# Optimization experiments

Hardware: AMD Instinct MI355X
Metric: run time of the kernel (lower is better)

## Reference

```python
import jax, jax.numpy as jnp
import numpy as np

B, T, D = 16, 512, 256
HS, D_A, R = 512, 64, 8


def setup_inputs() -> dict:
    key = jax.random.key(0)
    ks = jax.random.split(key, 8)
    s = lambda *sh: 1.0 / np.sqrt(sh[0])
    x = jax.random.normal(ks[0], (B, T, D), dtype=jnp.float32)
    w_first = jax.random.normal(ks[1], (D, D_A), dtype=jnp.float32) * s(D)
    b_first = jnp.zeros((D_A,), dtype=jnp.float32)
    w_second = jax.random.normal(ks[2], (D_A, R), dtype=jnp.float32) * s(D_A)
    b_second = jnp.zeros((R,), dtype=jnp.float32)
    weight_iBarh = jax.random.normal(ks[3], (D, 4 * HS), dtype=jnp.float32) * s(D)
    weight_hh = jax.random.normal(ks[4], (HS, 4 * HS), dtype=jnp.float32) * s(HS)
    bias = jnp.zeros((4 * HS,), dtype=jnp.float32)
    return {"x": x, "w_first": w_first, "b_first": b_first,
            "w_second": w_second, "b_second": b_second,
            "weight_iBarh": weight_iBarh, "weight_hh": weight_hh, "bias": bias}


def _forward(x, w_first, b_first, w_second, b_second, weight_iBarh, weight_hh, bias):
    b, t, d = x.shape
    hs = weight_hh.shape[0]
    r = w_second.shape[1]
    # attention logits for every timestep: (B, T, r)
    s = jnp.tanh(x @ w_first + b_first) @ w_second + b_second
    # causal mask: query t attends to keys j <= t
    mask = jnp.tril(jnp.ones((t, t), dtype=bool))  # (t_query, j_key)
    # logits: (B, Tq, Tk, r); softmax over key axis per (t, r), masked to prefix
    logits = jnp.where(mask[None, :, :, None], s[:, None, :, :], -jnp.inf)
    attn = jax.nn.softmax(logits, axis=2).mean(axis=-1)  # (B, Tq, Tk) == mean over r
    # M_t = attention-weighted average of prefix inputs: (B, T, D)
    M = jnp.einsum('btj,bjd->btd', attn, x)
    gates_x = jnp.einsum('btd,dg->btg', M, weight_iBarh) + bias  # (B, T, 4H)

    def step(carry, gx):
        h, c = carry
        g = gx + h @ weight_hh  # (B, 4H)
        i = jax.nn.sigmoid(g[:, :hs])
        f = jax.nn.sigmoid(g[:, hs:2 * hs])
        gg = jnp.tanh(g[:, 2 * hs:3 * hs])
        o = jax.nn.sigmoid(g[:, 3 * hs:])
        c = f * c + i * gg
        h = o * jnp.tanh(c)
        return (h, c), h

    h0 = jnp.zeros((b, hs), dtype=x.dtype)
    c0 = jnp.zeros((b, hs), dtype=x.dtype)
    (h_t, c_t), hseq = jax.lax.scan(step, (h0, c0), jnp.swapaxes(gates_x, 0, 1))
    hidden_seq = jnp.swapaxes(hseq, 0, 1)  # (B, T, H)
    return hidden_seq, h_t, c_t


def reference(x, w_first, b_first, w_second, b_second, weight_iBarh, weight_hh, bias):
    return _forward(x, w_first, b_first, w_second, b_second, weight_iBarh, weight_hh, bias)
```

## Files before the change

kernel.cpp:

```cpp
#include <hip/hip_runtime.h>
#include <math.h>

#define BB 16
#define TT 512
#define DD 256
#define HS 512
#define DA 64
#define RR 8
#define G4H 2048

typedef __attribute__((ext_vector_type(2))) float f2;
typedef __attribute__((ext_vector_type(8))) short bf16x8;
typedef __attribute__((ext_vector_type(4))) float f32x4;
typedef unsigned short ushort_t;


__device__ __forceinline__ ushort_t f2bf(float f) {
  const unsigned u = __float_as_uint(f);
  return (ushort_t)((u + 0x7FFFu + ((u >> 16) & 1u)) >> 16);
}

__global__ __launch_bounds__(256) void k0w_transpose(
    const float* __restrict__ W, ushort_t* __restrict__ Wt) {
  __shared__ float tl[64][65];
  const int kb = (blockIdx.x & 3) * 64;
  const int nb = (blockIdx.x >> 2) * 64;
  const int tid = threadIdx.x;
  for (int i = tid; i < 4096; i += 256)
    tl[i >> 6][i & 63] = W[(kb + (i >> 6)) * 2048 + nb + (i & 63)];
  __syncthreads();
  for (int i = tid; i < 4096; i += 256) {
    const int n = i >> 6, k = i & 63;
    Wt[(nb + n) * 256 + kb + k] = f2bf(tl[k][n]);
  }
}

__global__ __launch_bounds__(256) void k1_score(
    const float* __restrict__ x, const float* __restrict__ w1,
    const float* __restrict__ b1, const float* __restrict__ w2,
    const float* __restrict__ b2, float* __restrict__ s_out) {
  const int wave = threadIdx.x >> 6;
  const int lane = threadIdx.x & 63;
  for (int i = 0; i < 4; ++i) {
    const int bt = blockIdx.x * 16 + wave * 4 + i;
    const float* xr = x + bt * DD;
    float acc = b1[lane];
    #pragma unroll 4
    for (int d = 0; d < DD; ++d)
      acc = fmaf(xr[d], w1[d * DA + lane], acc);
    const float a = tanhf(acc);
    #pragma unroll
    for (int r = 0; r < RR; ++r) {
      float v = a * w2[lane * RR + r];
      for (int off = 32; off > 0; off >>= 1) v += __shfl_xor(v, off);
      if (lane == 0) s_out[bt * RR + r] = v + b2[r];
    }
  }
}

__global__ __launch_bounds__(512) void k2_prefix(
    const float* __restrict__ s_in, float* __restrict__ e_out,
    float* __restrict__ inv_out) {
  const int b = blockIdx.x >> 3, r = blockIdx.x & 7;
  const int t = threadIdx.x;
  __shared__ float red[TT];
  __shared__ float buf[2][TT];
  const float v = s_in[(b * TT + t) * RR + r];
  red[t] = v;
  __syncthreads();
  for (int off = 256; off >= 1; off >>= 1) {
    if (t < off) red[t] = fmaxf(red[t], red[t + off]);
    __syncthreads();
  }
  const float m = red[0];
  const float e = expf(v - m);
  int p = 0;
  buf[0][t] = e;
  __syncthreads();
  for (int off = 1; off < TT; off <<= 1) {
    const float add = (t >= off) ? buf[p][t - off] : 0.f;
    buf[1 - p][t] = buf[p][t] + add;
    __syncthreads();
    p ^= 1;
  }
  const float den = buf[p][t];
  e_out[(b * TT + t) * RR + r] = e;
  inv_out[(b * TT + t) * RR + r] = 1.0f / den;
}

__global__ __launch_bounds__(64) void k3_mix(
    const float* __restrict__ x, const float* __restrict__ e_in,
    const float* __restrict__ inv_in, ushort_t* __restrict__ Mout) {
  const int b = blockIdx.x >> 2;
  const int d = (blockIdx.x & 3) * 64 + threadIdx.x;
  __shared__ __align__(16) float el[TT * RR];
  __shared__ __align__(16) float il[TT * RR];
  for (int i = threadIdx.x * 4; i < TT * RR; i += 64 * 4) {
    *(float4*)&el[i] = *(const float4*)&e_in[b * TT * RR + i];
    *(float4*)&il[i] = *(const float4*)&inv_in[b * TT * RR + i];
  }
  __syncthreads();
  const float* xp = x + (long)b * TT * DD + d;
  float xv_c = xp[0];
  float xv_n = xp[DD];
  float4 c0 = {0.f, 0.f, 0.f, 0.f}, c1 = {0.f, 0.f, 0.f, 0.f};
  for (int t = 0; t < TT; ++t) {
    const float xv_f = (t + 2 < TT) ? xp[(t + 2) * DD] : 0.f;
    const float4 e0 = *(const float4*)&el[t * RR];
    const float4 e1 = *(const float4*)&el[t * RR + 4];
    const float4 i0 = *(const float4*)&il[t * RR];
    const float4 i1 = *(const float4*)&il[t * RR + 4];
    c0.x = fmaf(e0.x, xv_c, c0.x); c0.y = fmaf(e0.y, xv_c, c0.y);
    c0.z = fmaf(e0.z, xv_c, c0.z); c0.w = fmaf(e0.w, xv_c, c0.w);
    c1.x = fmaf(e1.x, xv_c, c1.x); c1.y = fmaf(e1.y, xv_c, c1.y);
    c1.z = fmaf(e1.z, xv_c, c1.z); c1.w = fmaf(e1.w, xv_c, c1.w);
    float msum = c0.x * i0.x + c0.y * i0.y + c0.z * i0.z + c0.w * i0.w;
    msum += c1.x * i1.x + c1.y * i1.y + c1.z * i1.z + c1.w * i1.w;
    Mout[(b * TT + t) * DD + d] = f2bf(msum * 0.125f);
    xv_c = xv_n;
    xv_n = xv_f;
  }
}

__global__ __launch_bounds__(256) void k4_mfma(
    const ushort_t* __restrict__ Mb, const ushort_t* __restrict__ Wtb,
    const float* __restrict__ bias, float* __restrict__ C) {
  const int bn = blockIdx.x & 15;
  const int bm = blockIdx.x >> 4;
  const int tid = threadIdx.x;
  const int wv = tid >> 6, lane = tid & 63;
  const int quad = lane >> 4, l16 = lane & 15;
  const int wm = (wv & 1) * 64, wn = (wv >> 1) * 64;
  const int row0 = bm * 128, col0 = bn * 128;

  __shared__ __align__(16) ushort_t As[128][40];
  __shared__ __align__(16) ushort_t Bs[128][40];

  f32x4 acc[4][4];
  #pragma unroll
  for (int i = 0; i < 4; ++i)
    #pragma unroll
    for (int j = 0; j < 4; ++j) acc[i][j] = (f32x4){0.f, 0.f, 0.f, 0.f};

  const int r = tid >> 1, koff = (tid & 1) * 16;
  for (int k0 = 0; k0 < 256; k0 += 32) {
    const uint4 av0 = *(const uint4*)&Mb[(row0 + r) * 256 + k0 + koff];
    const uint4 av1 = *(const uint4*)&Mb[(row0 + r) * 256 + k0 + koff + 8];
    const uint4 bv0 = *(const uint4*)&Wtb[(col0 + r) * 256 + k0 + koff];
    const uint4 bv1 = *(const uint4*)&Wtb[(col0 + r) * 256 + k0 + koff + 8];
    __syncthreads();
    *(uint4*)&As[r][koff] = av0; *(uint4*)&As[r][koff + 8] = av1;
    *(uint4*)&Bs[r][koff] = bv0; *(uint4*)&Bs[r][koff + 8] = bv1;
    __syncthreads();
    bf16x8 af[4], bfr[4];
    #pragma unroll
    for (int mi = 0; mi < 4; ++mi)
      af[mi] = *(const bf16x8*)&As[wm + mi * 16 + l16][quad * 8];
    #pragma unroll
    for (int ni = 0; ni < 4; ++ni)
      bfr[ni] = *(const bf16x8*)&Bs[wn + ni * 16 + l16][quad * 8];
    #pragma unroll
    for (int mi = 0; mi < 4; ++mi)
      #pragma unroll
      for (int ni = 0; ni < 4; ++ni)
        acc[mi][ni] = __builtin_amdgcn_mfma_f32_16x16x32_bf16(
            af[mi], bfr[ni], acc[mi][ni], 0, 0, 0);
  }
  #pragma unroll
  for (int ni = 0; ni < 4; ++ni) {
    const int col = col0 + wn + ni * 16 + l16;
    const float bv = bias[col];
    #pragma unroll
    for (int mi = 0; mi < 4; ++mi) {
      #pragma unroll
      for (int rg = 0; rg < 4; ++rg) {
        const int row = row0 + wm + mi * 16 + quad * 4 + rg;
        C[(long)row * 2048 + col] = acc[mi][ni][rg] + bv;
      }
    }
  }
}

__device__ __forceinline__ float fast_sigmoid(float x) {
  return __builtin_amdgcn_rcpf(1.f + __expf(-x));
}
__device__ __forceinline__ float fast_tanh(float x) {
  const float xc = fmaxf(x, -30.f);
  const float e = __expf(-2.f * xc);
  return (1.f - e) * __builtin_amdgcn_rcpf(1.f + e);
}

__device__ __forceinline__ unsigned long long poll_ld(
    const unsigned long long* p) {
  return __hip_atomic_load(p, __ATOMIC_RELAXED, __HIP_MEMORY_SCOPE_AGENT);
}

__global__ __launch_bounds__(512, 1) void k5_lstm(
    const float* __restrict__ gates, const float* __restrict__ whh,
    float* __restrict__ out, unsigned long long* hbuf) {
  const int s   = blockIdx.x & 15;
  const int b   = blockIdx.x >> 4;
  const int tid = threadIdx.x;
  const int kq  = tid & 15;
  const int cq  = tid >> 4;
  const int j0  = s * 32;
  const int unit = j0 + cq;
  const int slot = (tid >> 5) * 36 + (tid & 31);

  __shared__ __align__(16) float Wl[256 * 128];
  __shared__ __align__(16) float hl[2][576];

  f2 wrA[32], wrB[32];
  for (int rnd = 0; rnd < 2; ++rnd) {
    for (int i = tid * 4; i < 256 * 128; i += 512 * 4) {
      const int k = i >> 7, c = i & 127;
      *(float4*)&Wl[i] =
          *(const float4*)&whh[(rnd * 256 + k) * G4H + (c >> 5) * HS + j0 + (c & 31)];
    }
    __syncthreads();
    if ((kq >> 3) == rnd) {
      const int kb = (kq & 7) * 32;
      #pragma unroll
      for (int kk = 0; kk < 32; ++kk) {
        const int base = (kb + kk) * 128 + cq;
        wrA[kk].x = *(volatile const float*)&Wl[base];
        wrA[kk].y = *(volatile const float*)&Wl[base + 32];
        wrB[kk].x = *(volatile const float*)&Wl[base + 64];
        wrB[kk].y = *(volatile const float*)&Wl[base + 96];
      }
    }
    __syncthreads();
  }

  float c_reg = 0.f;

  float4 g_cur = {0, 0, 0, 0}, g_n1 = {0, 0, 0, 0};
  const float* gbase = gates + (long)b * TT * G4H + unit;
  if (kq < 2) {
    g_cur.x = gbase[0];            g_cur.y = gbase[HS];
    g_cur.z = gbase[2 * HS];       g_cur.w = gbase[3 * HS];
    const float* g1 = gbase + G4H;
    g_n1.x = g1[0];                g_n1.y = g1[HS];
    g_n1.z = g1[2 * HS];           g_n1.w = g1[3 * HS];
  }

  for (int t = 0; t < TT; ++t) {
    const int par = t & 1;
    if (t > 0) {
      const unsigned long long* ha =
          hbuf + (((t - 1) & 1) * BB + b) * HS + tid;
      unsigned long long p0 = poll_ld(ha);
      unsigned long long p1 = poll_ld(ha);
      while ((unsigned)(p0 >> 32) < (unsigned)t) {
        p0 = p1;
        p1 = poll_ld(ha);
      }
      hl[par][slot] = __uint_as_float((unsigned)p0);
    }
    float4 g_n2 = {0, 0, 0, 0};
    if (kq < 2) {
      const int tn = (t + 2 < TT) ? t + 2 : TT - 1;
      const float* g2 = gbase + (long)tn * G4H;
      g_n2.x = g2[0];        g_n2.y = g2[HS];
      g_n2.z = g2[2 * HS];   g_n2.w = g2[3 * HS];
    }
    __asm__ __volatile__("s_waitcnt lgkmcnt(0)\ns_barrier" ::: "memory");
    f2 acc01 = {0.f, 0.f}, acc23 = {0.f, 0.f};
    if (t > 0) {
      const float* hb = &hl[par][kq * 36];
      #pragma unroll
      for (int i = 0; i < 8; ++i) {
        const float4 h4 = *(const float4*)(hb + i * 4);
        const f2 hx = {h4.x, h4.x}, hy = {h4.y, h4.y};
        const f2 hz = {h4.z, h4.z}, hw = {h4.w, h4.w};
        acc01 += wrA[i * 4 + 0] * hx;  acc23 += wrB[i * 4 + 0] * hx;
        acc01 += wrA[i * 4 + 1] * hy;  acc23 += wrB[i * 4 + 1] * hy;
        acc01 += wrA[i * 4 + 2] * hz;  acc23 += wrB[i * 4 + 2] * hz;
        acc01 += wrA[i * 4 + 3] * hw;  acc23 += wrB[i * 4 + 3] * hw;
      }
    }
    #pragma unroll
    for (int off = 1; off <= 8; off <<= 1) {
      acc01.x += __shfl_xor(acc01.x, off);
      acc01.y += __shfl_xor(acc01.y, off);
      acc23.x += __shfl_xor(acc23.x, off);
      acc23.y += __shfl_xor(acc23.y, off);
    }
    if (kq < 2) {
      const float I = fast_sigmoid(acc01.x + g_cur.x);
      const float F = fast_sigmoid(acc01.y + g_cur.y);
      const float G = fast_tanh(acc23.x + g_cur.z);
      const float O = fast_sigmoid(acc23.y + g_cur.w);
      c_reg = F * c_reg + I * G;
      const float h = O * fast_tanh(c_reg);
      if (kq == 0) {
        const unsigned long long pkt =
            ((unsigned long long)(unsigned)(t + 1) << 32) |
            (unsigned long long)__float_as_uint(h);
        __hip_atomic_store(&hbuf[(par * BB + b) * HS + unit], pkt,
                           __ATOMIC_RELAXED, __HIP_MEMORY_SCOPE_AGENT);
      } else {
        out[((long)b * TT + t) * HS + unit] = h;
        if (t == TT - 1) {
          out[(long)BB * TT * HS + b * HS + unit] = h;
          out[(long)BB * TT * HS + BB * HS + b * HS + unit] = c_reg;
        }
      }
    }
    g_cur = g_n1;
    g_n1 = g_n2;
  }
}

extern "C" void kernel_launch(void* const* d_in, const int* in_sizes, int n_in,
                              void* d_out, int out_size, void* d_ws,
                              size_t ws_size, hipStream_t stream) {
  const float* x    = (const float*)d_in[0];
  const float* w1   = (const float*)d_in[1];
  const float* b1   = (const float*)d_in[2];
  const float* w2   = (const float*)d_in[3];
  const float* b2   = (const float*)d_in[4];
  const float* wih  = (const float*)d_in[5];
  const float* whh  = (const float*)d_in[6];
  const float* bias = (const float*)d_in[7];
  float* out = (float*)d_out;

  float* ws = (float*)d_ws;
  float* s_buf  = ws;
  float* e_buf  = ws + 65536;
  float* i_buf  = ws + 131072;
  ushort_t* Mb  = (ushort_t*)(ws + 196608);
  ushort_t* Wtb = (ushort_t*)(ws + 1245184);
  float* g_buf  = ws + 2293760;
  unsigned long long* hbuf64 = (unsigned long long*)ws;

  k0w_transpose<<<128, 256, 0, stream>>>(wih, Wtb);
  k1_score<<<512, 256, 0, stream>>>(x, w1, b1, w2, b2, s_buf);
  k2_prefix<<<BB * RR, 512, 0, stream>>>(s_buf, e_buf, i_buf);
  k3_mix<<<64, 64, 0, stream>>>(x, e_buf, i_buf, Mb);
  k4_mfma<<<64 * 16, 256, 0, stream>>>(Mb, Wtb, bias, g_buf);
  hipMemsetAsync(hbuf64, 0, 2 * BB * HS * sizeof(unsigned long long), stream);
  k5_lstm<<<256, 512, 0, stream>>>(g_buf, whh, out, hbuf64);
}
```

Before: 1.213 ms.

## Add L2-scoped fast polling path for LSTM hidden-state exchange with fallback

Adds a second hidden-state buffer that is polled with an sc0 global load, which is expected to be served from the local L2 instead of the device-coherent path. If a block fails to observe progress within a bounded number of tries, it permanently falls back to the existing agent-scope atomic poll. The block index mapping is swapped so that blocks sharing a batch are spread differently across XCDs. Lane kq==1's output-write duty moves onto lane kq==0, which now also writes both buffers. The fast path relies on writers and readers sharing an L2, and it can cost up to 768 wasted polls per step before the fallback kicks in.

Result: slower. 1.736 ms (+43.1%).

```diff
diff --git a/kernel.cpp b/kernel.cpp
--- a/kernel.cpp
+++ b/kernel.cpp
@@ -13,6 +13,7 @@
 typedef __attribute__((ext_vector_type(8))) short bf16x8;
 typedef __attribute__((ext_vector_type(4))) float f32x4;
 typedef unsigned short ushort_t;
+typedef unsigned long long u64;
 
 
 __device__ __forceinline__ ushort_t f2bf(float f) {
@@ -190,16 +191,22 @@
   return (1.f - e) * __builtin_amdgcn_rcpf(1.f + e);
 }
 
-__device__ __forceinline__ unsigned long long poll_ld(
-    const unsigned long long* p) {
+__device__ __forceinline__ u64 poll_ld(const u64* p) {
   return __hip_atomic_load(p, __ATOMIC_RELAXED, __HIP_MEMORY_SCOPE_AGENT);
+}
+
+__device__ __forceinline__ u64 l2_poll(const u64* p) {
+  u64 v;
+  asm volatile("global_load_dwordx2 %0, %1, off sc0\ns_waitcnt vmcnt(0)"
+               : "=&v"(v) : "v"(p) : "memory");
+  return v;
 }
 
 __global__ __launch_bounds__(512, 1) void k5_lstm(
     const float* __restrict__ gates, const float* __restrict__ whh,
-    float* __restrict__ out, unsigned long long* hbuf) {
-  const int s   = blockIdx.x & 15;
-  const int b   = blockIdx.x >> 4;
+    float* __restrict__ out, u64* hbuf, u64* hbuf_l2) {
+  const int s   = blockIdx.x >> 4;
+  const int b   = blockIdx.x & 15;
   const int tid = threadIdx.x;
   const int kq  = tid & 15;
   const int cq  = tid >> 4;
@@ -233,10 +240,11 @@
   }
 
   float c_reg = 0.f;
+  bool use_fast = true;
 
   float4 g_cur = {0, 0, 0, 0}, g_n1 = {0, 0, 0, 0};
   const float* gbase = gates + (long)b * TT * G4H + unit;
-  if (kq < 2) {
+  if (kq == 0) {
     g_cur.x = gbase[0];            g_cur.y = gbase[HS];
     g_cur.z = gbase[2 * HS];       g_cur.w = gbase[3 * HS];
     const float* g1 = gbase + G4H;
@@ -247,18 +255,28 @@
   for (int t = 0; t < TT; ++t) {
     const int par = t & 1;
     if (t > 0) {
-      const unsigned long long* ha =
-          hbuf + (((t - 1) & 1) * BB + b) * HS + tid;
-      unsigned long long p0 = poll_ld(ha);
-      unsigned long long p1 = poll_ld(ha);
-      while ((unsigned)(p0 >> 32) < (unsigned)t) {
-        p0 = p1;
-        p1 = poll_ld(ha);
-      }
-      hl[par][slot] = __uint_as_float((unsigned)p0);
+      const int pidx = (((t - 1) & 1) * BB + b) * HS + tid;
+      u64 pkt = 0;
+      bool got = false;
+      if (use_fast) {
+        const u64* ap = hbuf_l2 + pidx;
+        int tries = 768;
+        do {
+          pkt = l2_poll(ap);
+          if ((unsigned)(pkt >> 32) >= (unsigned)t) { got = true; break; }
+        } while (--tries);
+        if (!got) use_fast = false;
+      }
+      if (!got) {
+        const u64* ha = hbuf + pidx;
+        do {
+          pkt = poll_ld(ha);
+        } while ((unsigned)(pkt >> 32) < (unsigned)t);
+      }
+      hl[par][slot] = __uint_as_float((unsigned)pkt);
     }
     float4 g_n2 = {0, 0, 0, 0};
-    if (kq < 2) {
+    if (kq == 0) {
       const int tn = (t + 2 < TT) ? t + 2 : TT - 1;
       const float* g2 = gbase + (long)tn * G4H;
       g_n2.x = g2[0];        g_n2.y = g2[HS];
@@ -286,25 +304,23 @@
       acc23.x += __shfl_xor(acc23.x, off);
       acc23.y += __shfl_xor(acc23.y, off);
     }
-    if (kq < 2) {
+    if (kq == 0) {
       const float I = fast_sigmoid(acc01.x + g_cur.x);
       const float F = fast_sigmoid(acc01.y + g_cur.y);
       const float G = fast_tanh(acc23.x + g_cur.z);
       const float O = fast_sigmoid(acc23.y + g_cur.w);
       c_reg = F * c_reg + I * G;
       const float h = O * fast_tanh(c_reg);
-      if (kq == 0) {
-        const unsigned long long pkt =
-            ((unsigned long long)(unsigned)(t + 1) << 32) |
-            (unsigned long long)__float_as_uint(h);
-        __hip_atomic_store(&hbuf[(par * BB + b) * HS + unit], pkt,
-                           __ATOMIC_RELAXED, __HIP_MEMORY_SCOPE_AGENT);
-      } else {
-        out[((long)b * TT + t) * HS + unit] = h;
-        if (t == TT - 1) {
-          out[(long)BB * TT * HS + b * HS + unit] = h;
-          out[(long)BB * TT * HS + BB * HS + b * HS + unit] = c_reg;
-        }
+      const u64 pkt = ((u64)(unsigned)(t + 1) << 32) |
+                      (u64)__float_as_uint(h);
+      const int widx = (par * BB + b) * HS + unit;
+      hbuf_l2[widx] = pkt;
+      __hip_atomic_store(&hbuf[widx], pkt, __ATOMIC_RELAXED,
+                         __HIP_MEMORY_SCOPE_AGENT);
+      out[((long)b * TT + t) * HS + unit] = h;
+      if (t == TT - 1) {
+        out[(long)BB * TT * HS + b * HS + unit] = h;
+        out[(long)BB * TT * HS + BB * HS + b * HS + unit] = c_reg;
       }
     }
     g_cur = g_n1;
@@ -332,13 +348,14 @@
   ushort_t* Mb  = (ushort_t*)(ws + 196608);
   ushort_t* Wtb = (ushort_t*)(ws + 1245184);
   float* g_buf  = ws + 2293760;
-  unsigned long long* hbuf64 = (unsigned long long*)ws;
+  u64* hbuf_llc = (u64*)ws;
+  u64* hbuf_l2  = (u64*)(ws + 32768);
 
   k0w_transpose<<<128, 256, 0, stream>>>(wih, Wtb);
   k1_score<<<512, 256, 0, stream>>>(x, w1, b1, w2, b2, s_buf);
   k2_prefix<<<BB * RR, 512, 0, stream>>>(s_buf, e_buf, i_buf);
   k3_mix<<<64, 64, 0, stream>>>(x, e_buf, i_buf, Mb);
   k4_mfma<<<64 * 16, 256, 0, stream>>>(Mb, Wtb, bias, g_buf);
-  hipMemsetAsync(hbuf64, 0, 2 * BB * HS * sizeof(unsigned long long), stream);
-  k5_lstm<<<256, 512, 0, stream>>>(g_buf, whh, out, hbuf64);
-}
+  hipMemsetAsync(hbuf_llc, 0, 4 * BB * HS * sizeof(u64), stream);
+  k5_lstm<<<256, 512, 0, stream>>>(g_buf, whh, out, hbuf_llc, hbuf_l2);
+}
```
